# Performance work log

Hardware: AMD Instinct MI355X
Metric: run time of the kernel (lower is better)

Reference implementation:

```python
import jax, jax.numpy as jnp
import numpy as np

N_NODES = 50000
EPS_BN = 1e-5


def _glorot(key, shape):
    fan_in, fan_out = shape[0], shape[1]
    lim = jnp.sqrt(6.0 / (fan_in + fan_out))
    return jax.random.uniform(key, shape, jnp.float32, -lim, lim)


def setup_inputs() -> dict:
    key = jax.random.key(0)
    ks = jax.random.split(key, 12)
    x = jax.random.normal(ks[0], (N_NODES, 128), jnp.float32)
    y = jax.random.normal(ks[1], (256, 1), jnp.float32)
    edge_index = jax.random.randint(ks[2], (2, 800000), 0, N_NODES, jnp.int64)
    return {
        "x": x,
        "y": y,
        "edge_index": edge_index,
        # GCNConv weights (in_dim, out_dim) + bias
        "W1": _glorot(ks[3], (128, 128)), "b1": jnp.zeros((128,), jnp.float32),
        "W2": _glorot(ks[4], (128, 128)), "b2": jnp.zeros((128,), jnp.float32),
        "W3": _glorot(ks[5], (128, 64)),  "b3": jnp.zeros((64,), jnp.float32),
        # target MLP: BatchNorm1d(1) -> Linear(1,128) -> ReLU -> Dropout -> Linear(128,64)
        "bn_gamma": jnp.ones((1,), jnp.float32), "bn_beta": jnp.zeros((1,), jnp.float32),
        "Wm1": _glorot(ks[6], (1, 128)),  "bm1": jnp.zeros((128,), jnp.float32),
        "Wm2": _glorot(ks[7], (128, 64)), "bm2": jnp.zeros((64,), jnp.float32),
    }


def gcn_conv(h, W, b, src, dst, deg_isqrt, n):
    # PyG GCNConv: x' = D^-1/2 (A+I) D^-1/2 (x W) + b, self-loops included in src/dst
    h = h @ W  # [n, out]
    norm = (deg_isqrt[src] * deg_isqrt[dst])[:, None]  # [E, 1]
    msg = h[src] * norm  # gather + scale, [E, out]
    out = jax.ops.segment_sum(msg, dst, num_segments=n)  # scatter-add
    return out + b


def reference(x, y, edge_index, W1, b1, W2, b2, W3, b3, bn_gamma, bn_beta, Wm1, bm1, Wm2, bm2):
    n = x.shape[0]
    loops = jnp.arange(n, dtype=edge_index.dtype)
    src = jnp.concatenate([edge_index[0], loops])
    dst = jnp.concatenate([edge_index[1], loops])
    deg = jax.ops.segment_sum(jnp.ones_like(dst, dtype=x.dtype), dst, num_segments=n)
    deg_isqrt = jnp.where(deg > 0, jax.lax.rsqrt(deg), 0.0)

    h = jax.nn.relu(gcn_conv(x, W1, b1, src, dst, deg_isqrt, n))
    h = jax.nn.relu(gcn_conv(h, W2, b2, src, dst, deg_isqrt, n))
    h = gcn_conv(h, W3, b3, src, dst, deg_isqrt, n)
    # transform_feat: normalize per-node embeddings (global_mean_pool result is discarded in source)
    x_emb = h / jnp.clip(jnp.linalg.norm(h, axis=1, keepdims=True), 1e-12)

    # target branch: BatchNorm1d (training-mode batch stats), Linear, ReLU, Dropout(eval=id), Linear
    mu = jnp.mean(y, axis=0, keepdims=True)
    var = jnp.var(y, axis=0, keepdims=True)
    yb = (y - mu) * jax.lax.rsqrt(var + EPS_BN) * bn_gamma + bn_beta
    t = jax.nn.relu(yb @ Wm1 + bm1)
    t = t @ Wm2 + bm2
    y_emb = t / jnp.clip(jnp.linalg.norm(t, axis=1, keepdims=True), 1e-12)
    return (x_emb, y_emb)
```

## Files before the change

kernel.cpp:

```cpp
#include <hip/hip_runtime.h>
#include <hip/hip_bf16.h>

typedef __attribute__((ext_vector_type(8))) short short8;
typedef __attribute__((ext_vector_type(4))) float f32x4;

__device__ __forceinline__ ushort f2bf(float f) {
    union { float f; uint u; } v; v.f = f;
    uint u = v.u;
    return (ushort)((u + 0x7fffu + ((u >> 16) & 1u)) >> 16);
}
__device__ __forceinline__ float bf_lo(uint u) { return __uint_as_float(u << 16); }
__device__ __forceinline__ float bf_hi(uint u) { return __uint_as_float(u & 0xffff0000u); }
__device__ __forceinline__ float lane_bcast_f(float v, int j) {
    return __uint_as_float(__builtin_amdgcn_readlane(__float_as_uint(v), j));
}

#define PCHUNK 4096

__global__ __launch_bounds__(256) void k_partition(const int* __restrict__ src,
                                                   const int* __restrict__ dst, int E,
                                                   int nbuck, int cap,
                                                   int* __restrict__ gcur,
                                                   uint* __restrict__ part) {
    __shared__ int hist[256];
    __shared__ int base[256];
    __shared__ int cnt2[256];
    const int tid = threadIdx.x;
    const int s0 = blockIdx.x * PCHUNK;
    const int send = min(s0 + PCHUNK, E);
    hist[tid] = 0;
    cnt2[tid] = 0;
    __syncthreads();
    for (int i = s0 + tid; i < send; i += 256) {
        int d = dst[i];
        atomicAdd(&hist[d >> 8], 1);
    }
    __syncthreads();
    if (tid < nbuck && hist[tid] > 0) base[tid] = atomicAdd(&gcur[tid], hist[tid]);
    __syncthreads();
    for (int i = s0 + tid; i < send; i += 256) {
        int d = dst[i];
        int s = src[i];
        int k = d >> 8;
        int r = base[k] + atomicAdd(&cnt2[k], 1);
        if (r < cap) part[(size_t)k * cap + r] = ((uint)d << 16) | (uint)s;
    }
}

__global__ __launch_bounds__(256) void k_bucket_sort(const uint* __restrict__ part,
                                                     const int* __restrict__ gcur,
                                                     int nbuck, int cap, int n,
                                                     int* __restrict__ rowptr,
                                                     float* __restrict__ dis,
                                                     int* __restrict__ csr) {
    __shared__ int hist[256];
    __shared__ int pfx[256];
    __shared__ int sscan[256];
    const int b = blockIdx.x;
    const int tid = threadIdx.x;

    int gv = (tid < nbuck) ? min(gcur[tid], cap) : 0;
    sscan[tid] = gv;
    __syncthreads();
    for (int off = 1; off < 256; off <<= 1) {
        int t = (tid >= off) ? sscan[tid - off] : 0;
        __syncthreads();
        sscan[tid] += t;
        __syncthreads();
    }
    const int outbase = (b == 0) ? 0 : sscan[b - 1];
    const int sz = min(gcur[b], cap);
    const uint* seg = part + (size_t)b * cap;

    hist[tid] = 0;
    __syncthreads();
    for (int i = tid; i < sz; i += 256) atomicAdd(&hist[(seg[i] >> 16) & 255], 1);
    __syncthreads();

    int cnt_t = hist[tid];
    pfx[tid] = cnt_t;
    __syncthreads();
    for (int off = 1; off < 256; off <<= 1) {
        int t = (tid >= off) ? pfx[tid - off] : 0;
        __syncthreads();
        pfx[tid] += t;
        __syncthreads();
    }
    int excl = pfx[tid] - cnt_t;

    int node = b * 256 + tid;
    if (node < n) {
        rowptr[node] = outbase + excl;
        dis[node] = rsqrtf((float)(cnt_t + 1));
        if (node == n - 1) rowptr[n] = outbase + excl + cnt_t;
    }
    __syncthreads();
    pfx[tid] = excl;
    hist[tid] = 0;
    __syncthreads();
    for (int i = tid; i < sz; i += 256) {
        uint p = seg[i];
        int j = (p >> 16) & 255;
        int r = atomicAdd(&hist[j], 1);
        csr[outbase + pfx[j] + r] = (int)(p & 0xffffu);
    }
}

__global__ void k_wcast3(const float* __restrict__ W1, const float* __restrict__ W2,
                         const float* __restrict__ W3,
                         ushort* __restrict__ wt1, ushort* __restrict__ wt2,
                         ushort* __restrict__ wt3) {
    int i = blockIdx.x * 256 + threadIdx.x;
    if (i < 16384) {
        int k = i >> 7, nn = i & 127;
        wt1[nn * 128 + k] = f2bf(W1[i]);
    } else if (i < 32768) {
        int j = i - 16384;
        int k = j >> 7, nn = j & 127;
        wt2[nn * 128 + k] = f2bf(W2[j]);
    } else if (i < 40960) {
        int j = i - 32768;
        int k = j >> 6, nn = j & 63;
        wt3[nn * 128 + k] = f2bf(W3[j]);
    }
}

template <int COLS, bool F32IN>
__global__ __launch_bounds__(256) void gemm_mfma(const void* __restrict__ Xin,
                                                 const ushort* __restrict__ Wt,
                                                 ushort* __restrict__ Y, int n) {
    constexpr int LDW = 136;
    __shared__ ushort sX[64 * LDW];
    __shared__ ushort sW[COLS * LDW];
    const int tid = threadIdx.x;
    const int row0 = blockIdx.x * 64;

    if (F32IN) {
        const float* Xf = (const float*)Xin;
#pragma unroll
        for (int i = 0; i < 8; ++i) {
            int idx = i * 256 + tid;
            int r = idx >> 5, kc = idx & 31;
            int gr = min(row0 + r, n - 1);
            float4 v = *(const float4*)&Xf[(size_t)gr * 128 + kc * 4];
            ushort4 o;
            o.x = f2bf(v.x); o.y = f2bf(v.y); o.z = f2bf(v.z); o.w = f2bf(v.w);
            *(ushort4*)&sX[r * LDW + kc * 4] = o;
        }
    } else {
        const ushort* Xb = (const ushort*)Xin;
#pragma unroll
        for (int i = 0; i < 4; ++i) {
            int idx = i * 256 + tid;
            int r = idx >> 4, kc = idx & 15;
            int gr = min(row0 + r, n - 1);
            uint4 v = *(const uint4*)&Xb[(size_t)gr * 128 + kc * 8];
            *(uint4*)&sX[r * LDW + kc * 8] = v;
        }
    }
#pragma unroll
    for (int c = tid; c < COLS * 16; c += 256) {
        int r = c >> 4, kc = c & 15;
        uint4 v = *(const uint4*)&Wt[(size_t)r * 128 + kc * 8];
        *(uint4*)&sW[r * LDW + kc * 8] = v;
    }
    __syncthreads();

    constexpr int NT = (COLS == 128) ? 2 : 1;
    constexpr int WN = COLS / 4;
    const int w = tid >> 6;
    const int lane = tid & 63;
    const int lm = lane & 15;
    const int kq = lane >> 4;

    f32x4 acc[4][NT];
#pragma unroll
    for (int mt = 0; mt < 4; ++mt)
#pragma unroll
        for (int ntn = 0; ntn < NT; ++ntn) acc[mt][ntn] = (f32x4){0.f, 0.f, 0.f, 0.f};

#pragma unroll
    for (int ks = 0; ks < 4; ++ks) {
        const int k0 = ks * 32 + kq * 8;
        short8 bfr[NT];
#pragma unroll
        for (int ntn = 0; ntn < NT; ++ntn)
            bfr[ntn] = *(const short8*)&sW[(w * WN + ntn * 16 + lm) * LDW + k0];
#pragma unroll
        for (int mt = 0; mt < 4; ++mt) {
            short8 afr = *(const short8*)&sX[(mt * 16 + lm) * LDW + k0];
#pragma unroll
            for (int ntn = 0; ntn < NT; ++ntn)
                acc[mt][ntn] = __builtin_amdgcn_mfma_f32_16x16x32_bf16(afr, bfr[ntn], acc[mt][ntn], 0, 0, 0);
        }
    }

#pragma unroll
    for (int mt = 0; mt < 4; ++mt) {
        int r_base = row0 + mt * 16 + kq * 4;
#pragma unroll
        for (int ntn = 0; ntn < NT; ++ntn) {
            int col = w * WN + ntn * 16 + lm;
#pragma unroll
            for (int rr = 0; rr < 4; ++rr) {
                int r = r_base + rr;
                if (r < n) Y[(size_t)r * COLS + col] = f2bf(acc[mt][ntn][rr]);
            }
        }
    }
}

template <int COLS, bool RELU, bool NORM>
__global__ __launch_bounds__(256) void agg(const ushort* __restrict__ H,
                                           const float* __restrict__ dis,
                                           const int* __restrict__ rowptr,
                                           const int* __restrict__ csr,
                                           const float* __restrict__ bias,
                                           void* __restrict__ out, int n) {
    const int wid = blockIdx.x * 4 + (threadIdx.x >> 6);
    const int lane = threadIdx.x & 63;
    if (wid >= n) return;
    const int v = wid;
    const float dv = dis[v];
    const int e0 = rowptr[v];
    const int e1 = rowptr[v + 1];

    if (COLS == 128) {
        const uint* Hu = (const uint*)H;
        uint h0 = Hu[(size_t)v * 64 + lane];
        float ax = dv * bf_lo(h0), ay = dv * bf_hi(h0);

        int e = e0;
        while (e < e1) {
            const int c = min(e1 - e, 64);
            int sidx = 0; float sw = 0.0f;
            if (lane < c) { sidx = csr[e + lane]; sw = dis[sidx]; }
            int j = 0;
            for (; j + 16 <= c; j += 16) {
                uint hv[16]; float w[16];
#pragma unroll
                for (int u = 0; u < 16; ++u) {
                    int s = __builtin_amdgcn_readlane(sidx, j + u);
                    w[u] = lane_bcast_f(sw, j + u);
                    hv[u] = Hu[(size_t)s * 64 + lane];
                }
#pragma unroll
                for (int u = 0; u < 16; ++u) { ax += w[u] * bf_lo(hv[u]); ay += w[u] * bf_hi(hv[u]); }
            }
            for (; j + 4 <= c; j += 4) {
                uint hv[4]; float w[4];
#pragma unroll
                for (int u = 0; u < 4; ++u) {
                    int s = __builtin_amdgcn_readlane(sidx, j + u);
                    w[u] = lane_bcast_f(sw, j + u);
                    hv[u] = Hu[(size_t)s * 64 + lane];
                }
#pragma unroll
                for (int u = 0; u < 4; ++u) { ax += w[u] * bf_lo(hv[u]); ay += w[u] * bf_hi(hv[u]); }
            }
            for (; j < c; ++j) {
                int s = __builtin_amdgcn_readlane(sidx, j);
                float w = lane_bcast_f(sw, j);
                uint hh = Hu[(size_t)s * 64 + lane];
                ax += w * bf_lo(hh); ay += w * bf_hi(hh);
            }
            e += c;
        }

        float2 b = ((const float2*)bias)[lane];
        float rx = dv * ax + b.x;
        float ry = dv * ay + b.y;
        if (RELU) { rx = fmaxf(rx, 0.f); ry = fmaxf(ry, 0.f); }
        uint packed = (uint)f2bf(rx) | ((uint)f2bf(ry) << 16);
        ((uint*)out)[(size_t)v * 64 + lane] = packed;
    } else {
        float acc = dv * bf_lo((uint)H[(size_t)v * 64 + lane]);

        int e = e0;
        while (e < e1) {
            const int c = min(e1 - e, 64);
            int sidx = 0; float sw = 0.0f;
            if (lane < c) { sidx = csr[e + lane]; sw = dis[sidx]; }
            int j = 0;
            for (; j + 16 <= c; j += 16) {
                ushort hv[16]; float w[16];
#pragma unroll
                for (int u = 0; u < 16; ++u) {
                    int s = __builtin_amdgcn_readlane(sidx, j + u);
                    w[u] = lane_bcast_f(sw, j + u);
                    hv[u] = H[(size_t)s * 64 + lane];
                }
#pragma unroll
                for (int u = 0; u < 16; ++u) acc += w[u] * bf_lo((uint)hv[u]);
            }
            for (; j < c; ++j) {
                int s = __builtin_amdgcn_readlane(sidx, j);
                float w = lane_bcast_f(sw, j);
                acc += w * bf_lo((uint)H[(size_t)s * 64 + lane]);
            }
            e += c;
        }

        float r = dv * acc + bias[lane];
        if (RELU) r = fmaxf(r, 0.f);
        if (NORM) {
            float ss = r * r;
#pragma unroll
            for (int m = 1; m < 64; m <<= 1) ss += __shfl_xor(ss, m, 64);
            r = r / fmaxf(sqrtf(ss), 1e-12f);
        }
        ((float*)out)[(size_t)v * 64 + lane] = r;
    }
}

__global__ __launch_bounds__(256) void target_mlp(const float* __restrict__ y,
                                                  const float* __restrict__ gamma,
                                                  const float* __restrict__ beta,
                                                  const float* __restrict__ Wm1,
                                                  const float* __restrict__ bm1,
                                                  const float* __restrict__ Wm2,
                                                  const float* __restrict__ bm2,
                                                  float* __restrict__ out) {
    __shared__ float red[256];
    __shared__ float t1[128];
    __shared__ float s_mu, s_var;
    const int tid = threadIdx.x;
    float yv = y[tid];
    red[tid] = yv;
    __syncthreads();
    for (int s = 128; s > 0; s >>= 1) {
        if (tid < s) red[tid] += red[tid + s];
        __syncthreads();
    }
    if (tid == 0) s_mu = red[0] * (1.0f / 256.0f);
    __syncthreads();
    float mu = s_mu;
    float d = yv - mu;
    red[tid] = d * d;
    __syncthreads();
    for (int s = 128; s > 0; s >>= 1) {
        if (tid < s) red[tid] += red[tid + s];
        __syncthreads();
    }
    if (tid == 0) s_var = red[0] * (1.0f / 256.0f);
    __syncthreads();

    const int row = blockIdx.x;
    float yb = (y[row] - mu) * rsqrtf(s_var + 1e-5f) * gamma[0] + beta[0];
    if (tid < 128) t1[tid] = fmaxf(yb * Wm1[tid] + bm1[tid], 0.0f);
    __syncthreads();
    if (tid < 64) {
        float acc = bm2[tid];
#pragma unroll 8
        for (int c = 0; c < 128; ++c) acc += t1[c] * Wm2[c * 64 + tid];
        float ss = acc * acc;
#pragma unroll
        for (int m = 1; m < 64; m <<= 1) ss += __shfl_xor(ss, m, 64);
        out[row * 64 + tid] = acc / fmaxf(sqrtf(ss), 1e-12f);
    }
}

extern "C" void kernel_launch(void* const* d_in, const int* in_sizes, int n_in,
                              void* d_out, int out_size, void* d_ws, size_t ws_size,
                              hipStream_t stream) {
    const float* x     = (const float*)d_in[0];
    const float* y     = (const float*)d_in[1];
    const int*   edge  = (const int*)d_in[2];
    const float* W1    = (const float*)d_in[3];
    const float* b1    = (const float*)d_in[4];
    const float* W2    = (const float*)d_in[5];
    const float* b2    = (const float*)d_in[6];
    const float* W3    = (const float*)d_in[7];
    const float* b3    = (const float*)d_in[8];
    const float* bng   = (const float*)d_in[9];
    const float* bnb   = (const float*)d_in[10];
    const float* Wm1   = (const float*)d_in[11];
    const float* bm1   = (const float*)d_in[12];
    const float* Wm2   = (const float*)d_in[13];
    const float* bm2   = (const float*)d_in[14];

    const int n = in_sizes[0] / 128;
    const int E = in_sizes[2] / 2;
    const int* src = edge;
    const int* dst = edge + E;

    const int nbuck = (n + 255) / 256;
    const int cap = E / nbuck + E / nbuck / 4 + 1024;

    size_t off = 0;
    auto carve = [&](size_t bytes) {
        size_t p = off;
        off = (off + bytes + 255) & ~(size_t)255;
        return p;
    };
    char* ws = (char*)d_ws;
    int*    gcur    = (int*)(ws + carve(256 * 4));
    uint*   part    = (uint*)(ws + carve((size_t)nbuck * cap * 4));
    int*    rowptr  = (int*)(ws + carve((size_t)(n + 1) * 4));
    int*    csr     = (int*)(ws + carve((size_t)E * 4));
    float*  dis     = (float*)(ws + carve((size_t)n * 4));
    ushort* wt1     = (ushort*)(ws + carve(128 * 128 * 2));
    ushort* wt2     = (ushort*)(ws + carve(128 * 128 * 2));
    ushort* wt3     = (ushort*)(ws + carve(64 * 128 * 2));
    ushort* bufA    = (ushort*)(ws + carve((size_t)n * 128 * 2));
    ushort* bufB    = (ushort*)(ws + carve((size_t)n * 128 * 2));
    ushort* bufC    = (ushort*)(ws + carve((size_t)n * 64 * 2));
    (void)ws_size; (void)n_in; (void)out_size;

    float* x_emb = (float*)d_out;
    float* y_emb = (float*)d_out + (size_t)n * 64;

    hipMemsetAsync(gcur, 0, 256 * 4, stream);
    k_partition<<<(E + PCHUNK - 1) / PCHUNK, 256, 0, stream>>>(src, dst, E, nbuck, cap, gcur, part);
    k_bucket_sort<<<nbuck, 256, 0, stream>>>(part, gcur, nbuck, cap, n, rowptr, dis, csr);
    k_wcast3<<<160, 256, 0, stream>>>(W1, W2, W3, wt1, wt2, wt3);

    const int ggrid = (n + 63) / 64;
    const int agrid = (n + 3) / 4;

    gemm_mfma<128, true><<<ggrid, 256, 0, stream>>>(x, wt1, bufA, n);
    agg<128, true, false><<<agrid, 256, 0, stream>>>(bufA, dis, rowptr, csr, b1, bufB, n);
    gemm_mfma<128, false><<<ggrid, 256, 0, stream>>>(bufB, wt2, bufA, n);
    agg<128, true, false><<<agrid, 256, 0, stream>>>(bufA, dis, rowptr, csr, b2, bufB, n);
    gemm_mfma<64, false><<<ggrid, 256, 0, stream>>>(bufB, wt3, bufC, n);
    agg<64, false, true><<<agrid, 256, 0, stream>>>(bufC, dis, rowptr, csr, b3, x_emb, n);

    target_mlp<<<256, 256, 0, stream>>>(y, bng, bnb, Wm1, bm1, Wm2, bm2, y_emb);
}
```

Before: 268.7 us.

## Gather two neighbor rows per wavefront with wider loads and merge small kernels

After: 277.2 us. +3.2%, slower.

```diff
diff --git a/kernel.cpp b/kernel.cpp
--- a/kernel.cpp
+++ b/kernel.cpp
@@ -19,13 +19,37 @@
 
 __global__ __launch_bounds__(256) void k_partition(const int* __restrict__ src,
                                                    const int* __restrict__ dst, int E,
-                                                   int nbuck, int cap,
+                                                   int nbuck, int cap, int pblocks,
                                                    int* __restrict__ gcur,
-                                                   uint* __restrict__ part) {
+                                                   uint* __restrict__ part,
+                                                   const float* __restrict__ W1,
+                                                   const float* __restrict__ W2,
+                                                   const float* __restrict__ W3,
+                                                   ushort* __restrict__ wt1,
+                                                   ushort* __restrict__ wt2,
+                                                   ushort* __restrict__ wt3) {
     __shared__ int hist[256];
     __shared__ int base[256];
     __shared__ int cnt2[256];
     const int tid = threadIdx.x;
+
+    if ((int)blockIdx.x >= pblocks) {
+        int i = (blockIdx.x - pblocks) * 256 + tid;
+        if (i < 16384) {
+            int k = i >> 7, nn = i & 127;
+            wt1[nn * 128 + k] = f2bf(W1[i]);
+        } else if (i < 32768) {
+            int j = i - 16384;
+            int k = j >> 7, nn = j & 127;
+            wt2[nn * 128 + k] = f2bf(W2[j]);
+        } else if (i < 40960) {
+            int j = i - 32768;
+            int k = j >> 6, nn = j & 63;
+            wt3[nn * 128 + k] = f2bf(W3[j]);
+        }
+        return;
+    }
+
     const int s0 = blockIdx.x * PCHUNK;
     const int send = min(s0 + PCHUNK, E);
     hist[tid] = 0;
@@ -106,25 +130,6 @@
     }
 }
 
-__global__ void k_wcast3(const float* __restrict__ W1, const float* __restrict__ W2,
-                         const float* __restrict__ W3,
-                         ushort* __restrict__ wt1, ushort* __restrict__ wt2,
-                         ushort* __restrict__ wt3) {
-    int i = blockIdx.x * 256 + threadIdx.x;
-    if (i < 16384) {
-        int k = i >> 7, nn = i & 127;
-        wt1[nn * 128 + k] = f2bf(W1[i]);
-    } else if (i < 32768) {
-        int j = i - 16384;
-        int k = j >> 7, nn = j & 127;
-        wt2[nn * 128 + k] = f2bf(W2[j]);
-    } else if (i < 40960) {
-        int j = i - 32768;
-        int k = j >> 6, nn = j & 63;
-        wt3[nn * 128 + k] = f2bf(W3[j]);
-    }
-}
-
 template <int COLS, bool F32IN>
 __global__ __launch_bounds__(256) void gemm_mfma(const void* __restrict__ Xin,
                                                  const ushort* __restrict__ Wt,
@@ -210,13 +215,13 @@
     }
 }
 
-template <int COLS, bool RELU, bool NORM>
-__global__ __launch_bounds__(256) void agg(const ushort* __restrict__ H,
-                                           const float* __restrict__ dis,
-                                           const int* __restrict__ rowptr,
-                                           const int* __restrict__ csr,
-                                           const float* __restrict__ bias,
-                                           void* __restrict__ out, int n) {
+template <bool RELU>
+__global__ __launch_bounds__(256) void agg128(const ushort* __restrict__ H,
+                                              const float* __restrict__ dis,
+                                              const int* __restrict__ rowptr,
+                                              const int* __restrict__ csr,
+                                              const float* __restrict__ bias,
+                                              uint* __restrict__ out, int n) {
     const int wid = blockIdx.x * 4 + (threadIdx.x >> 6);
     const int lane = threadIdx.x & 63;
     if (wid >= n) return;
@@ -224,139 +229,204 @@
     const float dv = dis[v];
     const int e0 = rowptr[v];
     const int e1 = rowptr[v + 1];
-
-    if (COLS == 128) {
-        const uint* Hu = (const uint*)H;
-        uint h0 = Hu[(size_t)v * 64 + lane];
-        float ax = dv * bf_lo(h0), ay = dv * bf_hi(h0);
-
-        int e = e0;
-        while (e < e1) {
-            const int c = min(e1 - e, 64);
-            int sidx = 0; float sw = 0.0f;
-            if (lane < c) { sidx = csr[e + lane]; sw = dis[sidx]; }
-            int j = 0;
-            for (; j + 16 <= c; j += 16) {
-                uint hv[16]; float w[16];
-#pragma unroll
-                for (int u = 0; u < 16; ++u) {
-                    int s = __builtin_amdgcn_readlane(sidx, j + u);
-                    w[u] = lane_bcast_f(sw, j + u);
-                    hv[u] = Hu[(size_t)s * 64 + lane];
-                }
-#pragma unroll
-                for (int u = 0; u < 16; ++u) { ax += w[u] * bf_lo(hv[u]); ay += w[u] * bf_hi(hv[u]); }
+    const uint2* H2 = (const uint2*)H;
+    const int col = lane & 31;
+    const int half = lane >> 5;
+
+    float a0 = 0.f, a1 = 0.f, a2 = 0.f, a3 = 0.f;
+    int e = e0;
+    while (e < e1) {
+        const int c = min(e1 - e, 64);
+        int sidx = 0; float sw = 0.0f;
+        if (lane < c) { sidx = csr[e + lane]; sw = dis[sidx]; }
+        const int P = (c + 1) >> 1;
+        int p = 0;
+        for (; p + 8 <= P; p += 8) {
+            uint2 hv[8]; float w[8];
+#pragma unroll
+            for (int u = 0; u < 8; ++u) {
+                const int b2 = (p + u) * 2;
+                const int cs_o = min(b2 + 1, c - 1);
+                int s_e = __builtin_amdgcn_readlane(sidx, b2);
+                int s_o = __builtin_amdgcn_readlane(sidx, cs_o);
+                float w_e = lane_bcast_f(sw, b2);
+                float w_o = lane_bcast_f(sw, cs_o);
+                int s = half ? s_o : s_e;
+                float ww = half ? w_o : w_e;
+                w[u] = (b2 + half < c) ? ww : 0.0f;
+                hv[u] = H2[(size_t)s * 32 + col];
             }
-            for (; j + 4 <= c; j += 4) {
-                uint hv[4]; float w[4];
-#pragma unroll
-                for (int u = 0; u < 4; ++u) {
-                    int s = __builtin_amdgcn_readlane(sidx, j + u);
-                    w[u] = lane_bcast_f(sw, j + u);
-                    hv[u] = Hu[(size_t)s * 64 + lane];
-                }
-#pragma unroll
-                for (int u = 0; u < 4; ++u) { ax += w[u] * bf_lo(hv[u]); ay += w[u] * bf_hi(hv[u]); }
+#pragma unroll
+            for (int u = 0; u < 8; ++u) {
+                a0 += w[u] * bf_lo(hv[u].x); a1 += w[u] * bf_hi(hv[u].x);
+                a2 += w[u] * bf_lo(hv[u].y); a3 += w[u] * bf_hi(hv[u].y);
             }
-            for (; j < c; ++j) {
-                int s = __builtin_amdgcn_readlane(sidx, j);
-                float w = lane_bcast_f(sw, j);
-                uint hh = Hu[(size_t)s * 64 + lane];
-                ax += w * bf_lo(hh); ay += w * bf_hi(hh);
-            }
-            e += c;
-        }
-
-        float2 b = ((const float2*)bias)[lane];
-        float rx = dv * ax + b.x;
-        float ry = dv * ay + b.y;
-        if (RELU) { rx = fmaxf(rx, 0.f); ry = fmaxf(ry, 0.f); }
-        uint packed = (uint)f2bf(rx) | ((uint)f2bf(ry) << 16);
-        ((uint*)out)[(size_t)v * 64 + lane] = packed;
-    } else {
-        float acc = dv * bf_lo((uint)H[(size_t)v * 64 + lane]);
-
-        int e = e0;
-        while (e < e1) {
-            const int c = min(e1 - e, 64);
-            int sidx = 0; float sw = 0.0f;
-            if (lane < c) { sidx = csr[e + lane]; sw = dis[sidx]; }
-            int j = 0;
-            for (; j + 16 <= c; j += 16) {
-                ushort hv[16]; float w[16];
-#pragma unroll
-                for (int u = 0; u < 16; ++u) {
-                    int s = __builtin_amdgcn_readlane(sidx, j + u);
-                    w[u] = lane_bcast_f(sw, j + u);
-                    hv[u] = H[(size_t)s * 64 + lane];
-                }
-#pragma unroll
-                for (int u = 0; u < 16; ++u) acc += w[u] * bf_lo((uint)hv[u]);
-            }
-            for (; j < c; ++j) {
-                int s = __builtin_amdgcn_readlane(sidx, j);
-                float w = lane_bcast_f(sw, j);
-                acc += w * bf_lo((uint)H[(size_t)s * 64 + lane]);
-            }
-            e += c;
-        }
-
-        float r = dv * acc + bias[lane];
-        if (RELU) r = fmaxf(r, 0.f);
-        if (NORM) {
-            float ss = r * r;
-#pragma unroll
-            for (int m = 1; m < 64; m <<= 1) ss += __shfl_xor(ss, m, 64);
-            r = r / fmaxf(sqrtf(ss), 1e-12f);
-        }
-        ((float*)out)[(size_t)v * 64 + lane] = r;
-    }
-}
-
-__global__ __launch_bounds__(256) void target_mlp(const float* __restrict__ y,
-                                                  const float* __restrict__ gamma,
-                                                  const float* __restrict__ beta,
-                                                  const float* __restrict__ Wm1,
-                                                  const float* __restrict__ bm1,
-                                                  const float* __restrict__ Wm2,
-                                                  const float* __restrict__ bm2,
-                                                  float* __restrict__ out) {
+        }
+        for (; p < P; ++p) {
+            const int b2 = p * 2;
+            const int cs_o = min(b2 + 1, c - 1);
+            int s_e = __builtin_amdgcn_readlane(sidx, b2);
+            int s_o = __builtin_amdgcn_readlane(sidx, cs_o);
+            float w_e = lane_bcast_f(sw, b2);
+            float w_o = lane_bcast_f(sw, cs_o);
+            int s = half ? s_o : s_e;
+            float ww = half ? w_o : w_e;
+            float w0 = (b2 + half < c) ? ww : 0.0f;
+            uint2 hv = H2[(size_t)s * 32 + col];
+            a0 += w0 * bf_lo(hv.x); a1 += w0 * bf_hi(hv.x);
+            a2 += w0 * bf_lo(hv.y); a3 += w0 * bf_hi(hv.y);
+        }
+        e += c;
+    }
+    a0 += __shfl_xor(a0, 32, 64);
+    a1 += __shfl_xor(a1, 32, 64);
+    a2 += __shfl_xor(a2, 32, 64);
+    a3 += __shfl_xor(a3, 32, 64);
+
+    if (half == 0) {
+        uint2 hs = H2[(size_t)v * 32 + col];
+        float4 b = ((const float4*)bias)[col];
+        float d2 = dv * dv;
+        float r0 = dv * a0 + d2 * bf_lo(hs.x) + b.x;
+        float r1 = dv * a1 + d2 * bf_hi(hs.x) + b.y;
+        float r2 = dv * a2 + d2 * bf_lo(hs.y) + b.z;
+        float r3 = dv * a3 + d2 * bf_hi(hs.y) + b.w;
+        if (RELU) {
+            r0 = fmaxf(r0, 0.f); r1 = fmaxf(r1, 0.f);
+            r2 = fmaxf(r2, 0.f); r3 = fmaxf(r3, 0.f);
+        }
+        uint2 pk;
+        pk.x = (uint)f2bf(r0) | ((uint)f2bf(r1) << 16);
+        pk.y = (uint)f2bf(r2) | ((uint)f2bf(r3) << 16);
+        ((uint2*)out)[(size_t)v * 32 + col] = pk;
+    }
+}
+
+__global__ __launch_bounds__(256) void agg64_final(const ushort* __restrict__ H,
+                                                   const float* __restrict__ dis,
+                                                   const int* __restrict__ rowptr,
+                                                   const int* __restrict__ csr,
+                                                   const float* __restrict__ bias,
+                                                   float* __restrict__ out, int n, int agrid,
+                                                   const float* __restrict__ y,
+                                                   const float* __restrict__ gamma,
+                                                   const float* __restrict__ beta,
+                                                   const float* __restrict__ Wm1,
+                                                   const float* __restrict__ bm1,
+                                                   const float* __restrict__ Wm2,
+                                                   const float* __restrict__ bm2,
+                                                   float* __restrict__ out_y) {
     __shared__ float red[256];
     __shared__ float t1[128];
     __shared__ float s_mu, s_var;
     const int tid = threadIdx.x;
-    float yv = y[tid];
-    red[tid] = yv;
-    __syncthreads();
-    for (int s = 128; s > 0; s >>= 1) {
-        if (tid < s) red[tid] += red[tid + s];
-        __syncthreads();
-    }
-    if (tid == 0) s_mu = red[0] * (1.0f / 256.0f);
-    __syncthreads();
-    float mu = s_mu;
-    float d = yv - mu;
-    red[tid] = d * d;
-    __syncthreads();
-    for (int s = 128; s > 0; s >>= 1) {
-        if (tid < s) red[tid] += red[tid + s];
-        __syncthreads();
-    }
-    if (tid == 0) s_var = red[0] * (1.0f / 256.0f);
-    __syncthreads();
-
-    const int row = blockIdx.x;
-    float yb = (y[row] - mu) * rsqrtf(s_var + 1e-5f) * gamma[0] + beta[0];
-    if (tid < 128) t1[tid] = fmaxf(yb * Wm1[tid] + bm1[tid], 0.0f);
-    __syncthreads();
-    if (tid < 64) {
-        float acc = bm2[tid];
+
+    if ((int)blockIdx.x >= agrid) {
+        float yv = y[tid];
+        red[tid] = yv;
+        __syncthreads();
+        for (int s = 128; s > 0; s >>= 1) {
+            if (tid < s) red[tid] += red[tid + s];
+            __syncthreads();
+        }
+        if (tid == 0) s_mu = red[0] * (1.0f / 256.0f);
+        __syncthreads();
+        float mu = s_mu;
+        float d = yv - mu;
+        red[tid] = d * d;
+        __syncthreads();
+        for (int s = 128; s > 0; s >>= 1) {
+            if (tid < s) red[tid] += red[tid + s];
+            __syncthreads();
+        }
+        if (tid == 0) s_var = red[0] * (1.0f / 256.0f);
+        __syncthreads();
+
+        const int row = blockIdx.x - agrid;
+        float yb = (y[row] - mu) * rsqrtf(s_var + 1e-5f) * gamma[0] + beta[0];
+        if (tid < 128) t1[tid] = fmaxf(yb * Wm1[tid] + bm1[tid], 0.0f);
+        __syncthreads();
+        if (tid < 64) {
+            float acc = bm2[tid];
 #pragma unroll 8
-        for (int c = 0; c < 128; ++c) acc += t1[c] * Wm2[c * 64 + tid];
-        float ss = acc * acc;
-#pragma unroll
-        for (int m = 1; m < 64; m <<= 1) ss += __shfl_xor(ss, m, 64);
-        out[row * 64 + tid] = acc / fmaxf(sqrtf(ss), 1e-12f);
+            for (int c = 0; c < 128; ++c) acc += t1[c] * Wm2[c * 64 + tid];
+            float ss = acc * acc;
+#pragma unroll
+            for (int m = 1; m < 64; m <<= 1) ss += __shfl_xor(ss, m, 64);
+            out_y[row * 64 + tid] = acc / fmaxf(sqrtf(ss), 1e-12f);
+        }
+        return;
+    }
+
+    const int wid = blockIdx.x * 4 + (tid >> 6);
+    const int lane = tid & 63;
+    if (wid >= n) return;
+    const int v = wid;
+    const float dv = dis[v];
+    const int e0 = rowptr[v];
+    const int e1 = rowptr[v + 1];
+    const uint* Hu = (const uint*)H;
+    const int col = lane & 31;
+    const int half = lane >> 5;
+
+    float a0 = 0.f, a1 = 0.f;
+    int e = e0;
+    while (e < e1) {
+        const int c = min(e1 - e, 64);
+        int sidx = 0; float sw = 0.0f;
+        if (lane < c) { sidx = csr[e + lane]; sw = dis[sidx]; }
+        const int P = (c + 1) >> 1;
+        int p = 0;
+        for (; p + 8 <= P; p += 8) {
+            uint hv[8]; float w[8];
+#pragma unroll
+            for (int u = 0; u < 8; ++u) {
+                const int b2 = (p + u) * 2;
+                const int cs_o = min(b2 + 1, c - 1);
+                int s_e = __builtin_amdgcn_readlane(sidx, b2);
+                int s_o = __builtin_amdgcn_readlane(sidx, cs_o);
+                float w_e = lane_bcast_f(sw, b2);
+                float w_o = lane_bcast_f(sw, cs_o);
+                int s = half ? s_o : s_e;
+                float ww = half ? w_o : w_e;
+                w[u] = (b2 + half < c) ? ww : 0.0f;
+                hv[u] = Hu[(size_t)s * 32 + col];
+            }
+#pragma unroll
+            for (int u = 0; u < 8; ++u) {
+                a0 += w[u] * bf_lo(hv[u]); a1 += w[u] * bf_hi(hv[u]);
+            }
+        }
+        for (; p < P; ++p) {
+            const int b2 = p * 2;
+            const int cs_o = min(b2 + 1, c - 1);
+            int s_e = __builtin_amdgcn_readlane(sidx, b2);
+            int s_o = __builtin_amdgcn_readlane(sidx, cs_o);
+            float w_e = lane_bcast_f(sw, b2);
+            float w_o = lane_bcast_f(sw, cs_o);
+            int s = half ? s_o : s_e;
+            float ww = half ? w_o : w_e;
+            float w0 = (b2 + half < c) ? ww : 0.0f;
+            uint hv = Hu[(size_t)s * 32 + col];
+            a0 += w0 * bf_lo(hv); a1 += w0 * bf_hi(hv);
+        }
+        e += c;
+    }
+    a0 += __shfl_xor(a0, 32, 64);
+    a1 += __shfl_xor(a1, 32, 64);
+
+    if (half == 0) {
+        uint hs = Hu[(size_t)v * 32 + col];
+        float2 b = ((const float2*)bias)[col];
+        float d2 = dv * dv;
+        float r0 = dv * a0 + d2 * bf_lo(hs) + b.x;
+        float r1 = dv * a1 + d2 * bf_hi(hs) + b.y;
+        float ss = r0 * r0 + r1 * r1;
+#pragma unroll
+        for (int m = 1; m < 32; m <<= 1) ss += __shfl_xor(ss, m, 64);
+        float inv = 1.0f / fmaxf(sqrtf(ss), 1e-12f);
+        float2 o = make_float2(r0 * inv, r1 * inv);
+        ((float2*)out)[(size_t)v * 32 + col] = o;
     }
 }
 
@@ -410,20 +480,21 @@
     float* x_emb = (float*)d_out;
     float* y_emb = (float*)d_out + (size_t)n * 64;
 
+    const int pblocks = (E + PCHUNK - 1) / PCHUNK;
+
     hipMemsetAsync(gcur, 0, 256 * 4, stream);
-    k_partition<<<(E + PCHUNK - 1) / PCHUNK, 256, 0, stream>>>(src, dst, E, nbuck, cap, gcur, part);
+    k_partition<<<pblocks + 160, 256, 0, stream>>>(src, dst, E, nbuck, cap, pblocks,
+                                                   gcur, part, W1, W2, W3, wt1, wt2, wt3);
     k_bucket_sort<<<nbuck, 256, 0, stream>>>(part, gcur, nbuck, cap, n, rowptr, dis, csr);
-    k_wcast3<<<160, 256, 0, stream>>>(W1, W2, W3, wt1, wt2, wt3);
 
     const int ggrid = (n + 63) / 64;
     const int agrid = (n + 3) / 4;
 
     gemm_mfma<128, true><<<ggrid, 256, 0, stream>>>(x, wt1, bufA, n);
-    agg<128, true, false><<<agrid, 256, 0, stream>>>(bufA, dis, rowptr, csr, b1, bufB, n);
+    agg128<true><<<agrid, 256, 0, stream>>>(bufA, dis, rowptr, csr, b1, (uint*)bufB, n);
     gemm_mfma<128, false><<<ggrid, 256, 0, stream>>>(bufB, wt2, bufA, n);
-    agg<128, true, false><<<agrid, 256, 0, stream>>>(bufA, dis, rowptr, csr, b2, bufB, n);
+    agg128<true><<<agrid, 256, 0, stream>>>(bufA, dis, rowptr, csr, b2, (uint*)bufB, n);
     gemm_mfma<64, false><<<ggrid, 256, 0, stream>>>(bufB, wt3, bufC, n);
-    agg<64, false, true><<<agrid, 256, 0, stream>>>(bufC, dis, rowptr, csr, b3, x_emb, n);
-
-    target_mlp<<<256, 256, 0, stream>>>(y, bng, bnb, Wm1, bm1, Wm2, bm2, y_emb);
-}
+    agg64_final<<<agrid + 256, 256, 0, stream>>>(bufC, dis, rowptr, csr, b3, x_emb, n, agrid,
+                                                 y, bng, bnb, Wm1, bm1, Wm2, bm2, y_emb);
+}
```
